# Kernel tuning notes

Measured on AMD Instinct MI355X. Metric: run time of the kernel, lower is better.

The kernel has to match this reference:

```python
import jax, jax.numpy as jnp
import numpy as np
from jax import lax

B, N, C = 16, 16384, 90      # batch, anchors, classes
K = 100                      # per-class pre-NMS top-k
MAX_DET = 100                # final detections per image
IOU_THR = 0.5
SCORE_THR = 0.05


def setup_inputs() -> dict:
    key = jax.random.key(0)
    k1, k2, k3, k4 = jax.random.split(key, 4)
    box_encodings = jax.random.normal(k1, (B, N, 4), dtype=jnp.float32) * 0.5
    class_logits = jax.random.normal(k2, (B, N, C), dtype=jnp.float32) * 2.0 - 3.0
    # anchors as [ymin,xmin,ymax,xmax] in normalized coords
    centers = jax.random.uniform(k3, (N, 2), dtype=jnp.float32)             # (cy,cx)
    sizes = jax.random.uniform(k4, (N, 2), dtype=jnp.float32, minval=0.05, maxval=0.3)
    anchors = jnp.concatenate([centers - sizes / 2, centers + sizes / 2], axis=-1)
    return {"box_encodings": box_encodings, "class_logits": class_logits, "anchors": anchors}


def decode_boxes(enc, anchors):
    ymin, xmin, ymax, xmax = [anchors[:, i] for i in range(4)]
    ha, wa = ymax - ymin, xmax - xmin
    cya, cxa = (ymin + ymax) / 2, (xmin + xmax) / 2
    ty, tx, th, tw = enc[..., 0] / 10.0, enc[..., 1] / 10.0, enc[..., 2] / 5.0, enc[..., 3] / 5.0
    cy = ty * ha + cya
    cx = tx * wa + cxa
    h = jnp.exp(th) * ha
    w = jnp.exp(tw) * wa
    boxes = jnp.stack([cy - h / 2, cx - w / 2, cy + h / 2, cx + w / 2], axis=-1)
    return jnp.clip(boxes, 0.0, 1.0)  # [..., N, 4]


def pairwise_iou(b):  # b: [K,4]
    area = jnp.maximum(b[:, 2] - b[:, 0], 0) * jnp.maximum(b[:, 3] - b[:, 1], 0)
    iy = jnp.maximum(jnp.minimum(b[:, None, 2], b[None, :, 2]) - jnp.maximum(b[:, None, 0], b[None, :, 0]), 0)
    ix = jnp.maximum(jnp.minimum(b[:, None, 3], b[None, :, 3]) - jnp.maximum(b[:, None, 1], b[None, :, 1]), 0)
    inter = iy * ix
    union = area[:, None] + area[None, :] - inter
    return inter / jnp.maximum(union, 1e-8)


def nms_one_class(boxes, scores_c):  # boxes [N,4], scores_c [N]
    vals, idx = lax.top_k(scores_c, K)           # sorted descending
    bk = boxes[idx]                               # [K,4]
    iou = pairwise_iou(bk)                        # [K,K]
    def step(keep, i):
        supp = jnp.any(keep & (iou[i] >= IOU_THR))
        ki = (vals[i] > SCORE_THR) & (~supp)
        return keep.at[i].set(ki), None
    keep, _ = lax.scan(step, jnp.zeros((K,), bool), jnp.arange(K))
    return bk, vals * keep                        # suppressed -> score 0


def postprocess_one(boxes, scores):  # boxes [N,4], scores [N,C]
    bx_ck, sc_ck = jax.vmap(nms_one_class, in_axes=(None, 1))(boxes, scores)  # [C,K,4],[C,K]
    cls_ck = jnp.broadcast_to(jnp.arange(C, dtype=jnp.float32)[:, None], (C, K))
    sc_f = sc_ck.reshape(-1)
    fsc, fidx = lax.top_k(sc_f, MAX_DET)
    fbx = bx_ck.reshape(-1, 4)[fidx]
    fcl = cls_ck.reshape(-1)[fidx]
    return jnp.concatenate([fbx, fcl[:, None], fsc[:, None]], axis=-1)  # [MAX_DET, 6]


def reference(box_encodings, class_logits, anchors):
    boxes = decode_boxes(box_encodings, anchors)       # [B,N,4]
    scores = jax.nn.sigmoid(class_logits)              # [B,N,C]
    combined = jax.vmap(postprocess_one)(boxes, scores)  # [B,MAX_DET,6] = boxes|class|score
    return combined
```

## Files before the change

kernel.cpp:

```cpp
#include <hip/hip_runtime.h>
#include <stdint.h>
#include <math.h>

#define B_ 16
#define NN 16384
#define C_ 90
#define KSEL 100
#define MAXD 100
#define MFLAT (C_ * KSEL)
#define NPAIR 128
#define ZKEY 0x80000000u


__device__ __forceinline__ uint32_t fkey(float f) {
  uint32_t u = __float_as_uint(f);
  return (u & 0x80000000u) ? ~u : (u | 0x80000000u);
}
__device__ __forceinline__ float keyinv(uint32_t k) {
  uint32_t u = (k & 0x80000000u) ? (k & 0x7FFFFFFFu) : ~k;
  return __uint_as_float(u);
}

__device__ __forceinline__ uint32_t blockSum512(uint32_t v, uint32_t* red, uint32_t* s_total) {
  int tid = threadIdx.x;
#pragma unroll
  for (int o = 32; o > 0; o >>= 1) v += __shfl_down(v, o, 64);
  if ((tid & 63) == 0) red[tid >> 6] = v;
  __syncthreads();
  if (tid == 0) {
    uint32_t s = 0;
#pragma unroll
    for (int i = 0; i < 8; ++i) s += red[i];
    *s_total = s;
  }
  __syncthreads();
  return *s_total;
}

__global__ __launch_bounds__(256) void transpose_key16_kernel(const float* __restrict__ logits,
                                                              uint16_t* __restrict__ keys16T) {
  __shared__ uint32_t tile[128 * 91];
  int b = blockIdx.y;
  int n0 = blockIdx.x * 128;
  const float4* src4 = reinterpret_cast<const float4*>(logits + ((size_t)b * NN + n0) * C_);
  for (int p = threadIdx.x; p < 2880; p += 256) {
    float4 v = src4[p];
    int e = p * 4;
    float vv[4] = {v.x, v.y, v.z, v.w};
#pragma unroll
    for (int j = 0; j < 4; ++j) {
      int ee = e + j;
      tile[(ee / C_) * 91 + (ee % C_)] = fkey(vv[j]);
    }
  }
  __syncthreads();
  uint16_t* dstb = keys16T + (size_t)b * C_ * NN + n0;
  for (int q = threadIdx.x; q < C_ * 16; q += 256) {
    int c = q >> 4, g = q & 15;
    int nn2 = g * 8;
    uint4 o;
    o.x = (tile[(nn2 + 0) * 91 + c] >> 16) | (tile[(nn2 + 1) * 91 + c] & 0xFFFF0000u);
    o.y = (tile[(nn2 + 2) * 91 + c] >> 16) | (tile[(nn2 + 3) * 91 + c] & 0xFFFF0000u);
    o.z = (tile[(nn2 + 4) * 91 + c] >> 16) | (tile[(nn2 + 5) * 91 + c] & 0xFFFF0000u);
    o.w = (tile[(nn2 + 6) * 91 + c] >> 16) | (tile[(nn2 + 7) * 91 + c] & 0xFFFF0000u);
    reinterpret_cast<uint4*>(dstb + (size_t)c * NN)[g] = o;
  }
}

template <int TR>
__global__ __launch_bounds__(512, 4) void select_kernel(
    const uint16_t* __restrict__ keys16T,
    const float* __restrict__ logits,
    uint32_t* __restrict__ candPacked,
    uint32_t* __restrict__ candCount) {
  __shared__ uint32_t hist[2048];
  __shared__ uint32_t sc[512];
  __shared__ uint32_t ws8[64];
  __shared__ int s_bsel;
  __shared__ uint32_t s_Sincl, s_Sexcl;
  __shared__ uint32_t red[8];
  __shared__ uint32_t s_total;
  __shared__ uint32_t s_cnt;

  const int c = blockIdx.x, b = blockIdx.y;
  const int tid = threadIdx.x;

  uint32_t keyw[16];
  if (TR) {
    const uint4* src4 = reinterpret_cast<const uint4*>(keys16T + ((size_t)b * C_ + c) * NN);
#pragma unroll
    for (int q = 0; q < 4; ++q) {
      uint4 kv = src4[q * 512 + tid];
      keyw[4 * q + 0] = kv.x; keyw[4 * q + 1] = kv.y;
      keyw[4 * q + 2] = kv.z; keyw[4 * q + 3] = kv.w;
    }
  } else {
    const float* src = logits + (size_t)b * NN * C_ + c;
#pragma unroll
    for (int m = 0; m < 16; ++m) {
      uint32_t i0 = (uint32_t)((((m >> 2) * 512 + tid) * 8) + ((m & 3) * 2));
      uint32_t klo = fkey(src[(size_t)i0 * C_]) >> 16;
      uint32_t khi = fkey(src[(size_t)(i0 + 1) * C_]) >> 16;
      keyw[m] = klo | (khi << 16);
    }
  }

  reinterpret_cast<uint4*>(hist)[tid] = make_uint4(0u, 0u, 0u, 0u);
  __syncthreads();
#pragma unroll
  for (int m = 0; m < 16; ++m) {
    uint32_t w = keyw[m];
    atomicAdd(&hist[(w & 0xFFFFu) >> 5], 1u);
    atomicAdd(&hist[w >> 21], 1u);
  }
  __syncthreads();

  uint32_t m_above = 0;
  uint32_t need = 100u;
  uint32_t cut16 = 0;
  int found = 0;
  int tiepath = 0;
  uint32_t V16 = 0, Texact = NN - 1;

  {
    uint32_t h0 = hist[4 * tid], h1 = hist[4 * tid + 1];
    uint32_t h2 = hist[4 * tid + 2], h3 = hist[4 * tid + 3];
    sc[tid] = h0 + h1 + h2 + h3;
    if (tid == 0) s_bsel = -1;
    __syncthreads();
    if (tid < 64) {
      uint32_t w = 0;
      int base = tid * 8;
#pragma unroll
      for (int i = 0; i < 8; ++i) w += sc[base + i];
#pragma unroll
      for (int off = 1; off < 64; off <<= 1) {
        uint32_t v = __shfl_down(w, off, 64);
        if (tid + off < 64) w += v;
      }
      ws8[tid] = w;
    }
    __syncthreads();
    {
      int g = tid >> 3;
      uint32_t above = (g < 63) ? ws8[g + 1] : 0u;
      for (int j = (g << 3) + 7; j > tid; --j) above += sc[j];
      uint32_t run = above;
      int best = -1;
      uint32_t bi = 0, be = 0;
      uint32_t hh[4] = {h0, h1, h2, h3};
#pragma unroll
      for (int p = 3; p >= 0; --p) {
        uint32_t h = hh[p];
        run += h;
        if (best < 0 && run >= need) { best = 4 * tid + p; bi = run; be = run - h; }
      }
      if (best >= 0) atomicMax(&s_bsel, best);
      __syncthreads();
      if (best >= 0 && best == s_bsel) { s_Sincl = bi; s_Sexcl = be; }
    }
    __syncthreads();

    uint32_t bsel = (uint32_t)s_bsel;
    uint32_t Sincl = s_Sincl, Sexcl = s_Sexcl;
    if (Sincl <= (uint32_t)NPAIR) {
      cut16 = bsel << 5;
      found = 1;
    } else {
      m_above = Sexcl;
      need = 100u - m_above;
      __syncthreads();
      if (tid < 8) reinterpret_cast<uint4*>(hist)[tid] = make_uint4(0u, 0u, 0u, 0u);
      __syncthreads();
#pragma unroll
      for (int m = 0; m < 16; ++m) {
        uint32_t w = keyw[m];
        uint32_t klo = w & 0xFFFFu, khi = w >> 16;
        if ((klo >> 5) == bsel) atomicAdd(&hist[klo & 31u], 1u);
        if ((khi >> 5) == bsel) atomicAdd(&hist[khi & 31u], 1u);
      }
      __syncthreads();
      uint32_t run = 0;
      int b1 = -1;
      uint32_t Si = 0, Se = 0;
      for (int p = 31; p >= 0; --p) {
        uint32_t h = hist[p];
        run += h;
        if (b1 < 0 && run >= need) { b1 = p; Si = run; Se = run - h; }
      }
      uint32_t cutv = (bsel << 5) | (uint32_t)b1;
      if (m_above + Si <= (uint32_t)NPAIR) {
        cut16 = cutv;
        found = 1;
      } else {
        tiepath = 1;
        V16 = cutv;
        m_above += Se;
        uint32_t r = 100u - m_above;
        uint32_t lo2 = 0, hi2 = NN - 1;
        while (lo2 < hi2) {
          uint32_t mid2 = lo2 + ((hi2 - lo2) >> 1);
          uint32_t cnt = 0;
#pragma unroll
          for (int m = 0; m < 16; ++m) {
            uint32_t w = keyw[m];
            uint32_t i0 = (uint32_t)((((m >> 2) * 512 + tid) * 8) + ((m & 3) * 2));
            cnt += ((w & 0xFFFFu) == V16 && i0 <= mid2) ? 1u : 0u;
            cnt += ((w >> 16) == V16 && (i0 + 1) <= mid2) ? 1u : 0u;
          }
          uint32_t tot = blockSum512(cnt, red, &s_total);
          if (tot >= r) hi2 = mid2; else lo2 = mid2 + 1;
        }
        Texact = lo2;
      }
    }
  }

  if (tid == 0) s_cnt = 0;
  __syncthreads();
  uint32_t* outp = candPacked + (size_t)(b * C_ + c) * NPAIR;
#pragma unroll
  for (int m = 0; m < 16; ++m) {
    uint32_t w = keyw[m];
    uint32_t i0 = (uint32_t)((((m >> 2) * 512 + tid) * 8) + ((m & 3) * 2));
    uint32_t klo = w & 0xFFFFu, khi = w >> 16;
    bool t0 = tiepath ? (klo > V16 || (klo == V16 && i0 <= Texact)) : (klo >= cut16);
    bool t1 = tiepath ? (khi > V16 || (khi == V16 && (i0 + 1) <= Texact)) : (khi >= cut16);
    if (t0) {
      uint32_t p = atomicAdd(&s_cnt, 1u);
      if (p < (uint32_t)NPAIR) outp[p] = (klo << 16) | i0;
    }
    if (t1) {
      uint32_t p = atomicAdd(&s_cnt, 1u);
      if (p < (uint32_t)NPAIR) outp[p] = (khi << 16) | (i0 + 1);
    }
  }
  __syncthreads();
  if (tid == 0) candCount[b * C_ + c] = (s_cnt > (uint32_t)NPAIR) ? (uint32_t)NPAIR : s_cnt;
}

__global__ __launch_bounds__(128, 4) void sort_nms_kernel(
    const uint32_t* __restrict__ candPacked,
    const uint32_t* __restrict__ candCount,
    const float* __restrict__ logits,
    const float* __restrict__ enc,
    const float* __restrict__ anchors,
    float* __restrict__ candBox,
    float* __restrict__ candScore) {
  __shared__ unsigned long long ck[NPAIR];
  __shared__ float p_box[NPAIR][5];
  __shared__ float p_area[NPAIR];
  __shared__ float s_vals[KSEL];
  __shared__ float s_boxv[KSEL][5];
  __shared__ float s_area[KSEL];
  __shared__ uint32_t smask[KSEL][4];
  __shared__ unsigned long long s_keepw[2];

  const int c = blockIdx.x, b = blockIdx.y;
  const int tid = threadIdx.x;
  const int bc = b * C_ + c;

  uint32_t cnt = candCount[bc];
  bool valid = tid < (int)cnt;
  uint32_t v = candPacked[(size_t)bc * NPAIR + tid];
  int n = valid ? (int)(v & 0x3FFFu) : 0;

  float x = logits[((size_t)b * NN + n) * C_ + c];
  float4 e = reinterpret_cast<const float4*>(enc)[(size_t)b * NN + n];
  float4 a = reinterpret_cast<const float4*>(anchors)[n];

  float s = 1.0f / (1.0f + expf(-x));
  unsigned long long ckv = 0ull;
  if (valid)
    ckv = ((unsigned long long)fkey(s) << 32) |
          (unsigned long long)((((uint32_t)(NN - 1 - n)) << 7) | (uint32_t)tid);
  ck[tid] = ckv;

  {
    float ha = a.z - a.x, wa = a.w - a.y;
    float cya = (a.x + a.z) * 0.5f, cxa = (a.y + a.w) * 0.5f;
    float cy = (e.x / 10.0f) * ha + cya;
    float cx = (e.y / 10.0f) * wa + cxa;
    float h = expf(e.z / 5.0f) * ha;
    float w = expf(e.w / 5.0f) * wa;
    float y1 = fminf(fmaxf(cy - h * 0.5f, 0.0f), 1.0f);
    float x1 = fminf(fmaxf(cx - w * 0.5f, 0.0f), 1.0f);
    float y2 = fminf(fmaxf(cy + h * 0.5f, 0.0f), 1.0f);
    float x2 = fminf(fmaxf(cx + w * 0.5f, 0.0f), 1.0f);
    p_box[tid][0] = y1; p_box[tid][1] = x1; p_box[tid][2] = y2; p_box[tid][3] = x2;
    p_area[tid] = fmaxf(y2 - y1, 0.0f) * fmaxf(x2 - x1, 0.0f);
  }
  __syncthreads();

  for (int kk = 2; kk <= 128; kk <<= 1) {
    for (int j = kk >> 1; j > 0; j >>= 1) {
      int ixj = tid ^ j;
      if (ixj > tid) {
        unsigned long long aa = ck[tid], bb2 = ck[ixj];
        if ((aa < bb2) == ((tid & kk) == 0)) { ck[tid] = bb2; ck[ixj] = aa; }
      }
      __syncthreads();
    }
  }

  if (tid < KSEL) {
    unsigned long long keyv = ck[tid];
    int slot = (int)((uint32_t)keyv & 127u);
    s_vals[tid] = keyinv((uint32_t)(keyv >> 32));
    s_boxv[tid][0] = p_box[slot][0]; s_boxv[tid][1] = p_box[slot][1];
    s_boxv[tid][2] = p_box[slot][2]; s_boxv[tid][3] = p_box[slot][3];
    s_area[tid] = p_area[slot];
    smask[tid][0] = 0; smask[tid][1] = 0; smask[tid][2] = 0; smask[tid][3] = 0;
  }
  __syncthreads();

  for (int p = tid; p < (KSEL * (KSEL - 1)) / 2; p += 128) {
    int j = (int)((1.0f + sqrtf(1.0f + 8.0f * (float)p)) * 0.5f);
    while (j * (j - 1) / 2 > p) --j;
    while ((j + 1) * j / 2 <= p) ++j;
    int i = p - j * (j - 1) / 2;
    float iy1 = s_boxv[i][0], ix1 = s_boxv[i][1], iy2 = s_boxv[i][2], ix2 = s_boxv[i][3];
    float jy1 = s_boxv[j][0], jx1 = s_boxv[j][1], jy2 = s_boxv[j][2], jx2 = s_boxv[j][3];
    float ta = fmaxf(fminf(iy2, jy2) - fmaxf(iy1, jy1), 0.0f) *
               fmaxf(fminf(ix2, jx2) - fmaxf(ix1, jx1), 0.0f);
    float un = fmaxf(s_area[i] + s_area[j] - ta, 1e-8f);
    if (ta / un >= 0.5f) atomicOr(&smask[i][j >> 5], 1u << (j & 31));
  }
  __syncthreads();

  if (tid < 64) {
    int L = tid;
    unsigned long long r0 = (unsigned long long)smask[L][0] |
                            ((unsigned long long)smask[L][1] << 32);
    unsigned long long r1 = (unsigned long long)smask[L][2] |
                            ((unsigned long long)smask[L][3] << 32);
    unsigned long long r2 = 0, r3 = 0;
    if (L < KSEL - 64) {
      r2 = (unsigned long long)smask[L + 64][0] | ((unsigned long long)smask[L + 64][1] << 32);
      r3 = (unsigned long long)smask[L + 64][2] | ((unsigned long long)smask[L + 64][3] << 32);
    }
    unsigned long long vm0 = __ballot(s_vals[L] > 0.05f);
    unsigned long long vm1 = __ballot((L + 64 < KSEL) ? (s_vals[L + 64] > 0.05f) : false);
    unsigned long long supp0 = 0, supp1 = 0, k0 = 0, k1 = 0;
    for (int j = 0; j < KSEL; ++j) {
      unsigned long long rl, rh;
      bool pass;
      if (j < 64) {
        rl = __shfl(r0, j); rh = __shfl(r1, j);
        pass = ((vm0 >> j) & 1ull) && !((supp0 >> j) & 1ull);
      } else {
        rl = __shfl(r2, j - 64); rh = __shfl(r3, j - 64);
        pass = ((vm1 >> (j - 64)) & 1ull) && !((supp1 >> (j - 64)) & 1ull);
      }
      if (pass) {
        supp0 |= rl; supp1 |= rh;
        if (j < 64) k0 |= 1ull << j; else k1 |= 1ull << (j - 64);
      }
    }
    if (tid == 0) { s_keepw[0] = k0; s_keepw[1] = k1; }
  }
  __syncthreads();

  if (tid < KSEL) {
    bool kept = (tid < 64) ? ((s_keepw[0] >> tid) & 1ull)
                           : ((s_keepw[1] >> (tid - 64)) & 1ull);
    size_t base = (size_t)bc * KSEL + tid;
    candScore[base] = kept ? s_vals[tid] : 0.0f;
    float* cb = candBox + base * 4;
    cb[0] = s_boxv[tid][0]; cb[1] = s_boxv[tid][1];
    cb[2] = s_boxv[tid][2]; cb[3] = s_boxv[tid][3];
  }
}

#define FT_NT 512
#define FT_SLOTS 18
#define FT_NW 8
__global__ __launch_bounds__(FT_NT) void final_topk_kernel(
    const float* __restrict__ candScore,
    const float* __restrict__ candBox,
    float* __restrict__ out) {
  __shared__ uint32_t skey[FT_NT * FT_SLOTS];
  __shared__ uint32_t hist[FT_NW * 2048];
  __shared__ uint32_t sc[512];
  __shared__ uint32_t ws8[64];
  __shared__ int s_bsel;
  __shared__ uint32_t s_Sincl, s_Sexcl;
  __shared__ uint32_t red[8];
  __shared__ uint32_t s_total;
  __shared__ uint32_t s_cnt;
  __shared__ unsigned long long ck[128];

  int b = blockIdx.x, tid = threadIdx.x;
  const int wid = tid >> 6;
  const float* src = candScore + (size_t)b * MFLAT;

  uint32_t nzc = 0;
  for (int q = 0; q < FT_SLOTS; ++q) {
    int idx = q * FT_NT + tid;
    uint32_t k = (idx < MFLAT) ? fkey(src[idx]) : 0u;
    skey[idx] = k;
    nzc += (k > ZKEY) ? 1u : 0u;
  }
  __syncthreads();
  uint32_t nz = blockSum512(nzc, red, &s_total);

  uint32_t cutHi = 0, m_above = 0, cut32 = 0;
  int found = 0, tiepath = 0;
  uint32_t V32 = 0, Texact = (uint32_t)(MFLAT - 1);
  uint32_t tie_r = 0;

  if (nz < 100u) {
    tiepath = 1;
    V32 = ZKEY;
    tie_r = 100u - nz;
  } else {
    for (int lvl = 0; lvl < 3; ++lvl) {
      const int shiftLo = (lvl == 0) ? 21 : (lvl == 1) ? 10 : 0;
      const uint32_t mask = (lvl == 2) ? 0x3FFu : 0x7FFu;
      const int nbits = (lvl == 2) ? 10 : 11;

      for (int i = tid; i < FT_NW * 512; i += FT_NT)
        reinterpret_cast<uint4*>(hist)[i] = make_uint4(0u, 0u, 0u, 0u);
      __syncthreads();
      uint32_t* myh = hist + wid * 2048;
      for (int q = 0; q < FT_SLOTS; ++q) {
        uint32_t k = skey[q * FT_NT + tid];
        bool in = (k > ZKEY) && ((lvl == 0) ? true : ((k >> (shiftLo + nbits)) == cutHi));
        if (in) atomicAdd(&myh[(k >> shiftLo) & mask], 1u);
      }
      __syncthreads();

      const uint32_t need = 100u - m_above;

      uint32_t h0 = 0, h1 = 0, h2 = 0, h3 = 0;
#pragma unroll
      for (int w = 0; w < FT_NW; ++w) {
        uint4 a = *reinterpret_cast<const uint4*>(hist + w * 2048 + 4 * tid);
        h0 += a.x; h1 += a.y; h2 += a.z; h3 += a.w;
      }
      sc[tid] = h0 + h1 + h2 + h3;
      if (tid == 0) s_bsel = -1;
      __syncthreads();
      if (tid < 64) {
        uint32_t w = 0;
        int base = tid * 8;
#pragma unroll
        for (int i = 0; i < 8; ++i) w += sc[base + i];
#pragma unroll
        for (int off = 1; off < 64; off <<= 1) {
          uint32_t v = __shfl_down(w, off, 64);
          if (tid + off < 64) w += v;
        }
        ws8[tid] = w;
      }
      __syncthreads();
      {
        int g = tid >> 3;
        uint32_t above = (g < 63) ? ws8[g + 1] : 0u;
        for (int j = (g << 3) + 7; j > tid; --j) above += sc[j];
        uint32_t run = above;
        int best = -1;
        uint32_t bi = 0, be = 0;
        uint32_t hh[4] = {h0, h1, h2, h3};
#pragma unroll
        for (int p = 3; p >= 0; --p) {
          uint32_t h = hh[p];
          run += h;
          if (best < 0 && run >= need) { best = 4 * tid + p; bi = run; be = run - h; }
        }
        if (best >= 0) atomicMax(&s_bsel, best);
        __syncthreads();
        if (best >= 0 && best == s_bsel) { s_Sincl = bi; s_Sexcl = be; }
      }
      __syncthreads();

      uint32_t bsel = (uint32_t)s_bsel;
      cutHi = (cutHi << nbits) | bsel;
      if (m_above + s_Sincl <= 128u) {
        cut32 = cutHi << shiftLo;
        found = 1;
        break;
      }
      m_above += s_Sexcl;
      __syncthreads();
    }

    if (!found) {
      tiepath = 1;
      V32 = cutHi;
      tie_r = 100u - m_above;
    }
  }

  if (tiepath) {
    uint32_t lo2 = 0, hi2 = (uint32_t)(MFLAT - 1);
    while (lo2 < hi2) {
      uint32_t mid2 = lo2 + ((hi2 - lo2) >> 1);
      uint32_t cnt = 0;
      for (int q = 0; q < FT_SLOTS; ++q) {
        uint32_t idx = (uint32_t)(q * FT_NT + tid);
        cnt += (skey[idx] == V32 && idx <= mid2) ? 1u : 0u;
      }
      uint32_t tot = blockSum512(cnt, red, &s_total);
      if (tot >= tie_r) hi2 = mid2; else lo2 = mid2 + 1;
    }
    Texact = lo2;
  }

  if (tid == 0) s_cnt = 0;
  __syncthreads();
  for (int q = 0; q < FT_SLOTS; ++q) {
    uint32_t idx = (uint32_t)(q * FT_NT + tid);
    uint32_t k = skey[idx];
    bool take = tiepath ? (k > V32 || (k == V32 && idx <= Texact))
                        : (k > ZKEY && k >= cut32);
    if (take) {
      uint32_t p = atomicAdd(&s_cnt, 1u);
      if (p < 128u)
        ck[p] = ((unsigned long long)k << 32) | (unsigned long long)(~idx);
    }
  }
  __syncthreads();
  if (tid < 128 && (uint32_t)tid >= s_cnt) ck[tid] = 0ull;
  __syncthreads();

  for (int kk = 2; kk <= 128; kk <<= 1) {
    for (int j = kk >> 1; j > 0; j >>= 1) {
      if (tid < 128) {
        int ixj = tid ^ j;
        if (ixj > tid) {
          unsigned long long a = ck[tid], bb = ck[ixj];
          if ((a < bb) == ((tid & kk) == 0)) { ck[tid] = bb; ck[ixj] = a; }
        }
      }
      __syncthreads();
    }
  }

  if (tid < MAXD) {
    unsigned long long keyv = ck[tid];
    int f = (int)(~(uint32_t)(keyv & 0xFFFFFFFFull));
    int c = f / KSEL;
    float sc2 = keyinv((uint32_t)(keyv >> 32));
    const float* cb = candBox + ((size_t)b * MFLAT + f) * 4;
    float* o = out + ((size_t)b * MAXD + tid) * 6;
    o[0] = cb[0]; o[1] = cb[1]; o[2] = cb[2]; o[3] = cb[3];
    o[4] = (float)c; o[5] = sc2;
  }
}

extern "C" void kernel_launch(void* const* d_in, const int* in_sizes, int n_in,
                              void* d_out, int out_size, void* d_ws, size_t ws_size,
                              hipStream_t stream) {
  const float* enc = (const float*)d_in[0];
  const float* logits = (const float*)d_in[1];
  const float* anchors = (const float*)d_in[2];
  float* out = (float*)d_out;
  char* ws = (char*)d_ws;

  size_t off = 0;
  float* candBox = (float*)(ws + off);   off += (size_t)B_ * C_ * KSEL * 4 * sizeof(float);
  float* candScore = (float*)(ws + off); off += (size_t)B_ * C_ * KSEL * sizeof(float);
  uint32_t* candPacked = (uint32_t*)(ws + off);
  off += (size_t)B_ * C_ * NPAIR * sizeof(uint32_t);
  uint32_t* candCount = (uint32_t*)(ws + off); off += (size_t)B_ * C_ * sizeof(uint32_t);
  off = (off + 255) & ~(size_t)255;
  uint16_t* keys16T = (uint16_t*)(ws + off);
  size_t needT = off + (size_t)B_ * C_ * NN * sizeof(uint16_t);
  int transposed = (ws_size >= needT) ? 1 : 0;

  if (transposed) {
    transpose_key16_kernel<<<dim3(NN / 128, B_), 256, 0, stream>>>(logits, keys16T);
    select_kernel<1><<<dim3(C_, B_), 512, 0, stream>>>(keys16T, logits, candPacked, candCount);
  } else {
    select_kernel<0><<<dim3(C_, B_), 512, 0, stream>>>(keys16T, logits, candPacked, candCount);
  }

  sort_nms_kernel<<<dim3(C_, B_), 128, 0, stream>>>(candPacked, candCount, logits,
                                                    enc, anchors, candBox, candScore);

  final_topk_kernel<<<B_, FT_NT, 0, stream>>>(candScore, candBox, out);
}
```

Baseline: 135.5 us.

## Overlap IoU mask computation with bitonic sort using warp-specialized 256-thread blocks

The sort_nms kernel now runs 256 threads. The first half loads scores and runs the bitonic sort, while the second half decodes boxes and computes full 128x128 IoU masks in slot order, five columns per sort step. This takes the IoU pass off the critical path after the sort and drops the triangular index math and shared-memory atomics. The greedy NMS then walks sorted order through slot indirection. The cost is computing the full square of IoUs instead of the triangle, and doubling block size, which may reduce occupancy.

```diff
diff --git a/kernel.cpp b/kernel.cpp
--- a/kernel.cpp
+++ b/kernel.cpp
@@ -239,7 +239,7 @@
   if (tid == 0) candCount[b * C_ + c] = (s_cnt > (uint32_t)NPAIR) ? (uint32_t)NPAIR : s_cnt;
 }
 
-__global__ __launch_bounds__(128, 4) void sort_nms_kernel(
+__global__ __launch_bounds__(256, 4) void sort_nms_kernel(
     const uint32_t* __restrict__ candPacked,
     const uint32_t* __restrict__ candCount,
     const float* __restrict__ logits,
@@ -250,125 +250,113 @@
   __shared__ unsigned long long ck[NPAIR];
   __shared__ float p_box[NPAIR][5];
   __shared__ float p_area[NPAIR];
-  __shared__ float s_vals[KSEL];
-  __shared__ float s_boxv[KSEL][5];
-  __shared__ float s_area[KSEL];
-  __shared__ uint32_t smask[KSEL][4];
+  __shared__ float p_val[NPAIR];
+  __shared__ unsigned long long M[NPAIR][2];
   __shared__ unsigned long long s_keepw[2];
 
   const int c = blockIdx.x, b = blockIdx.y;
   const int tid = threadIdx.x;
   const int bc = b * C_ + c;
-
-  uint32_t cnt = candCount[bc];
-  bool valid = tid < (int)cnt;
-  uint32_t v = candPacked[(size_t)bc * NPAIR + tid];
-  int n = valid ? (int)(v & 0x3FFFu) : 0;
-
-  float x = logits[((size_t)b * NN + n) * C_ + c];
-  float4 e = reinterpret_cast<const float4*>(enc)[(size_t)b * NN + n];
-  float4 a = reinterpret_cast<const float4*>(anchors)[n];
-
-  float s = 1.0f / (1.0f + expf(-x));
-  unsigned long long ckv = 0ull;
-  if (valid)
-    ckv = ((unsigned long long)fkey(s) << 32) |
-          (unsigned long long)((((uint32_t)(NN - 1 - n)) << 7) | (uint32_t)tid);
-  ck[tid] = ckv;
-
-  {
+  const uint32_t cnt = candCount[bc];
+
+  float ry1 = 0, rx1 = 0, ry2 = 0, rx2 = 0, rar = 0;
+
+  if (tid < NPAIR) {
+    int s = tid;
+    uint32_t v = candPacked[(size_t)bc * NPAIR + s];
+    int n = (s < (int)cnt) ? (int)(v & 0x3FFFu) : 0;
+    float x = logits[((size_t)b * NN + n) * C_ + c];
+    float sv = 1.0f / (1.0f + expf(-x));
+    p_val[s] = sv;
+    unsigned long long ckv = 0ull;
+    if (s < (int)cnt)
+      ckv = ((unsigned long long)fkey(sv) << 32) |
+            (unsigned long long)((((uint32_t)(NN - 1 - n)) << 7) | (uint32_t)s);
+    ck[s] = ckv;
+  } else {
+    int s = tid - NPAIR;
+    uint32_t v = candPacked[(size_t)bc * NPAIR + s];
+    int n = (s < (int)cnt) ? (int)(v & 0x3FFFu) : 0;
+    float4 e = reinterpret_cast<const float4*>(enc)[(size_t)b * NN + n];
+    float4 a = reinterpret_cast<const float4*>(anchors)[n];
     float ha = a.z - a.x, wa = a.w - a.y;
     float cya = (a.x + a.z) * 0.5f, cxa = (a.y + a.w) * 0.5f;
     float cy = (e.x / 10.0f) * ha + cya;
     float cx = (e.y / 10.0f) * wa + cxa;
     float h = expf(e.z / 5.0f) * ha;
     float w = expf(e.w / 5.0f) * wa;
-    float y1 = fminf(fmaxf(cy - h * 0.5f, 0.0f), 1.0f);
-    float x1 = fminf(fmaxf(cx - w * 0.5f, 0.0f), 1.0f);
-    float y2 = fminf(fmaxf(cy + h * 0.5f, 0.0f), 1.0f);
-    float x2 = fminf(fmaxf(cx + w * 0.5f, 0.0f), 1.0f);
-    p_box[tid][0] = y1; p_box[tid][1] = x1; p_box[tid][2] = y2; p_box[tid][3] = x2;
-    p_area[tid] = fmaxf(y2 - y1, 0.0f) * fmaxf(x2 - x1, 0.0f);
-  }
-  __syncthreads();
-
+    ry1 = fminf(fmaxf(cy - h * 0.5f, 0.0f), 1.0f);
+    rx1 = fminf(fmaxf(cx - w * 0.5f, 0.0f), 1.0f);
+    ry2 = fminf(fmaxf(cy + h * 0.5f, 0.0f), 1.0f);
+    rx2 = fminf(fmaxf(cx + w * 0.5f, 0.0f), 1.0f);
+    rar = fmaxf(ry2 - ry1, 0.0f) * fmaxf(rx2 - rx1, 0.0f);
+    p_box[s][0] = ry1; p_box[s][1] = rx1; p_box[s][2] = ry2; p_box[s][3] = rx2;
+    p_area[s] = rar;
+  }
+  __syncthreads();
+
+  unsigned long long m0 = 0ull, m1 = 0ull;
+  int step = 0;
   for (int kk = 2; kk <= 128; kk <<= 1) {
     for (int j = kk >> 1; j > 0; j >>= 1) {
-      int ixj = tid ^ j;
-      if (ixj > tid) {
-        unsigned long long aa = ck[tid], bb2 = ck[ixj];
-        if ((aa < bb2) == ((tid & kk) == 0)) { ck[tid] = bb2; ck[ixj] = aa; }
-      }
-      __syncthreads();
-    }
-  }
+      if (tid < NPAIR) {
+        int ixj = tid ^ j;
+        if (ixj > tid) {
+          unsigned long long aa = ck[tid], bb2 = ck[ixj];
+          if ((aa < bb2) == ((tid & kk) == 0)) { ck[tid] = bb2; ck[ixj] = aa; }
+        }
+      } else {
+        int c0 = step * 5;
+#pragma unroll
+        for (int qq = 0; qq < 5; ++qq) {
+          int q = c0 + qq;
+          if (q < NPAIR) {
+            float iy1 = p_box[q][0], ix1 = p_box[q][1];
+            float iy2 = p_box[q][2], ix2 = p_box[q][3];
+            float ta = fmaxf(fminf(iy2, ry2) - fmaxf(iy1, ry1), 0.0f) *
+                       fmaxf(fminf(ix2, rx2) - fmaxf(ix1, rx1), 0.0f);
+            float un = fmaxf(p_area[q] + rar - ta, 1e-8f);
+            bool hit = (ta / un >= 0.5f);
+            if (q < 64) m0 |= (unsigned long long)hit << q;
+            else        m1 |= (unsigned long long)hit << (q - 64);
+          }
+        }
+      }
+      ++step;
+      __syncthreads();
+    }
+  }
+  if (tid >= NPAIR) {
+    int s = tid - NPAIR;
+    M[s][0] = m0; M[s][1] = m1;
+  }
+  __syncthreads();
+
+  if (tid < 64) {
+    unsigned long long supp0 = 0, supp1 = 0, k0 = 0, k1 = 0;
+    for (int j = 0; j < KSEL; ++j) {
+      int sl = (int)((uint32_t)ck[j] & 127u);
+      bool suppd = (sl < 64) ? ((supp0 >> sl) & 1ull) : ((supp1 >> (sl - 64)) & 1ull);
+      bool pass = (p_val[sl] > 0.05f) && !suppd;
+      if (pass) {
+        supp0 |= M[sl][0]; supp1 |= M[sl][1];
+        if (j < 64) k0 |= 1ull << j; else k1 |= 1ull << (j - 64);
+      }
+    }
+    if (tid == 0) { s_keepw[0] = k0; s_keepw[1] = k1; }
+  }
+  __syncthreads();
 
   if (tid < KSEL) {
     unsigned long long keyv = ck[tid];
     int slot = (int)((uint32_t)keyv & 127u);
-    s_vals[tid] = keyinv((uint32_t)(keyv >> 32));
-    s_boxv[tid][0] = p_box[slot][0]; s_boxv[tid][1] = p_box[slot][1];
-    s_boxv[tid][2] = p_box[slot][2]; s_boxv[tid][3] = p_box[slot][3];
-    s_area[tid] = p_area[slot];
-    smask[tid][0] = 0; smask[tid][1] = 0; smask[tid][2] = 0; smask[tid][3] = 0;
-  }
-  __syncthreads();
-
-  for (int p = tid; p < (KSEL * (KSEL - 1)) / 2; p += 128) {
-    int j = (int)((1.0f + sqrtf(1.0f + 8.0f * (float)p)) * 0.5f);
-    while (j * (j - 1) / 2 > p) --j;
-    while ((j + 1) * j / 2 <= p) ++j;
-    int i = p - j * (j - 1) / 2;
-    float iy1 = s_boxv[i][0], ix1 = s_boxv[i][1], iy2 = s_boxv[i][2], ix2 = s_boxv[i][3];
-    float jy1 = s_boxv[j][0], jx1 = s_boxv[j][1], jy2 = s_boxv[j][2], jx2 = s_boxv[j][3];
-    float ta = fmaxf(fminf(iy2, jy2) - fmaxf(iy1, jy1), 0.0f) *
-               fmaxf(fminf(ix2, jx2) - fmaxf(ix1, jx1), 0.0f);
-    float un = fmaxf(s_area[i] + s_area[j] - ta, 1e-8f);
-    if (ta / un >= 0.5f) atomicOr(&smask[i][j >> 5], 1u << (j & 31));
-  }
-  __syncthreads();
-
-  if (tid < 64) {
-    int L = tid;
-    unsigned long long r0 = (unsigned long long)smask[L][0] |
-                            ((unsigned long long)smask[L][1] << 32);
-    unsigned long long r1 = (unsigned long long)smask[L][2] |
-                            ((unsigned long long)smask[L][3] << 32);
-    unsigned long long r2 = 0, r3 = 0;
-    if (L < KSEL - 64) {
-      r2 = (unsigned long long)smask[L + 64][0] | ((unsigned long long)smask[L + 64][1] << 32);
-      r3 = (unsigned long long)smask[L + 64][2] | ((unsigned long long)smask[L + 64][3] << 32);
-    }
-    unsigned long long vm0 = __ballot(s_vals[L] > 0.05f);
-    unsigned long long vm1 = __ballot((L + 64 < KSEL) ? (s_vals[L + 64] > 0.05f) : false);
-    unsigned long long supp0 = 0, supp1 = 0, k0 = 0, k1 = 0;
-    for (int j = 0; j < KSEL; ++j) {
-      unsigned long long rl, rh;
-      bool pass;
-      if (j < 64) {
-        rl = __shfl(r0, j); rh = __shfl(r1, j);
-        pass = ((vm0 >> j) & 1ull) && !((supp0 >> j) & 1ull);
-      } else {
-        rl = __shfl(r2, j - 64); rh = __shfl(r3, j - 64);
-        pass = ((vm1 >> (j - 64)) & 1ull) && !((supp1 >> (j - 64)) & 1ull);
-      }
-      if (pass) {
-        supp0 |= rl; supp1 |= rh;
-        if (j < 64) k0 |= 1ull << j; else k1 |= 1ull << (j - 64);
-      }
-    }
-    if (tid == 0) { s_keepw[0] = k0; s_keepw[1] = k1; }
-  }
-  __syncthreads();
-
-  if (tid < KSEL) {
     bool kept = (tid < 64) ? ((s_keepw[0] >> tid) & 1ull)
                            : ((s_keepw[1] >> (tid - 64)) & 1ull);
     size_t base = (size_t)bc * KSEL + tid;
-    candScore[base] = kept ? s_vals[tid] : 0.0f;
+    candScore[base] = kept ? keyinv((uint32_t)(keyv >> 32)) : 0.0f;
     float* cb = candBox + base * 4;
-    cb[0] = s_boxv[tid][0]; cb[1] = s_boxv[tid][1];
-    cb[2] = s_boxv[tid][2]; cb[3] = s_boxv[tid][3];
+    cb[0] = p_box[slot][0]; cb[1] = p_box[slot][1];
+    cb[2] = p_box[slot][2]; cb[3] = p_box[slot][3];
   }
 }
 
@@ -576,7 +564,7 @@
     select_kernel<0><<<dim3(C_, B_), 512, 0, stream>>>(keys16T, logits, candPacked, candCount);
   }
 
-  sort_nms_kernel<<<dim3(C_, B_), 128, 0, stream>>>(candPacked, candCount, logits,
+  sort_nms_kernel<<<dim3(C_, B_), 256, 0, stream>>>(candPacked, candCount, logits,
                                                     enc, anchors, candBox, candScore);
 
   final_topk_kernel<<<B_, FT_NT, 0, stream>>>(candScore, candBox, out);
```

Measured after the change: 143.2 us. 5.7% more time.
